# Optimization experiments

Measured on AMD Instinct MI355X. Metric: run time of the kernel, lower is better.

Reference implementation:

```python
import jax, jax.numpy as jnp
import numpy as np

B, L, H = 4096, 4096, 1024  # batch, num_labels, hidden_size


def setup_inputs() -> dict:
    key = jax.random.key(0)
    k1, k2, k3, k4, k5 = jax.random.split(key, 5)
    return {
        "bert_output": jax.random.normal(k1, (B, H), dtype=jnp.float32),
        "label_embed": jax.random.normal(k2, (L, H), dtype=jnp.float32),
        "W": jax.random.normal(k3, (L, H), dtype=jnp.float32) * 0.02,
        "b": jax.random.normal(k4, (L,), dtype=jnp.float32) * 0.02,
        "labels": jax.random.randint(k5, (B, L), 0, 2, dtype=jnp.int32),
    }


def reference(bert_output, label_embed, W, b, labels):
    # Original: output[i, j] = classifier(bert_output[i] + label_embed[j])[j]
    #         = sum_k (x[i,k] + E[j,k]) * W[j,k] + b[j]
    #         = (x @ W^T)[i,j] + (E * W).sum(-1)[j] + b[j]
    xWt = jnp.einsum('bh,lh->bl', bert_output, W)          # [B, L] GEMM
    diag_bias = jnp.sum(label_embed * W, axis=-1) + b       # [L] epilogue
    logits = xWt + diag_bias[None, :]                       # [B, L]
    return logits
```

## Files before the change

kernel.cpp:

```cpp
#include <hip/hip_runtime.h>
#include <hip/hip_bf16.h>

#define Bdim 4096
#define Ldim 4096
#define Hdim 1024
#define TILE 128
#define BK 32

typedef __attribute__((ext_vector_type(8))) __bf16 bf16x8;
typedef __attribute__((ext_vector_type(4))) float floatx4;

__device__ __forceinline__ unsigned short f2bf(float f) {
  union { __hip_bfloat16 h; unsigned short u; } c;
  c.h = __float2bfloat16(f);
  return c.u;
}

__global__ __launch_bounds__(256) void prep_kernel(
    const float* __restrict__ X, const float* __restrict__ E,
    const float* __restrict__ W, const float* __restrict__ b,
    unsigned short* __restrict__ Xb, unsigned short* __restrict__ Wb,
    float* __restrict__ bias) {
  const int blk = blockIdx.x;
  const int t = threadIdx.x;
  if (blk < Ldim) {
    const int row = blk;
    const float4 wv = reinterpret_cast<const float4*>(W + (size_t)row * Hdim)[t];
    const float4 ev = reinterpret_cast<const float4*>(E + (size_t)row * Hdim)[t];
    ushort4 o;
    o.x = f2bf(wv.x); o.y = f2bf(wv.y); o.z = f2bf(wv.z); o.w = f2bf(wv.w);
    reinterpret_cast<ushort4*>(Wb + (size_t)row * Hdim)[t] = o;
    float dot = wv.x * ev.x + wv.y * ev.y + wv.z * ev.z + wv.w * ev.w;
#pragma unroll
    for (int off = 32; off > 0; off >>= 1) dot += __shfl_down(dot, off, 64);
    __shared__ float part[4];
    if ((t & 63) == 0) part[t >> 6] = dot;
    __syncthreads();
    if (t == 0) bias[row] = part[0] + part[1] + part[2] + part[3] + b[row];
  } else {
    const int i = (blk - Ldim) * 256 + t;
    float4 v = reinterpret_cast<const float4*>(X)[i];
    ushort4 o;
    o.x = f2bf(v.x); o.y = f2bf(v.y); o.z = f2bf(v.z); o.w = f2bf(v.w);
    reinterpret_cast<ushort4*>(Xb)[i] = o;
  }
}

__global__ __launch_bounds__(256) void gemm_bias_kernel(
    const unsigned short* __restrict__ A,
    const unsigned short* __restrict__ Bw,
    const float* __restrict__ bias,
    float* __restrict__ C) {
  __shared__ __align__(16) unsigned short ring[3][2][TILE * BK];

  const int tid = threadIdx.x;
  const int wave = tid >> 6;
  const int lane = tid & 63;
  const int m_blk = blockIdx.y * TILE;
  const int n_blk = blockIdx.x * TILE;

  const int srow = wave * 32 + (lane >> 2);
  const unsigned short* gA = A + (size_t)(m_blk + srow) * Hdim + (lane & 3) * 8;
  const unsigned short* gB = Bw + (size_t)(n_blk + srow) * Hdim + (lane & 3) * 8;
  const int lofs = wave * 32 * BK;

  const int wm = (wave >> 1) * 64;
  const int wn = (wave & 1) * 64;
  const int fr = lane & 15;
  const int fq = lane >> 4;
  const int fa = (wm + fr) * BK + fq * 8;
  const int fb = (wn + fr) * BK + fq * 8;

  floatx4 acc[4][4] = {};

#define GLL(src, dst)                                                  \
  __builtin_amdgcn_global_load_lds(                                    \
      (const __attribute__((address_space(1))) void*)(src),            \
      (__attribute__((address_space(3))) void*)(dst), 16, 0, 0)

#define STAGE(slot, kk)                                                \
  do {                                                                 \
    GLL(gA + (kk) * BK, &ring[slot][0][lofs]);                         \
    GLL(gA + (kk) * BK + 16 * Hdim, &ring[slot][0][lofs + 16 * BK]);   \
    GLL(gB + (kk) * BK, &ring[slot][1][lofs]);                         \
    GLL(gB + (kk) * BK + 16 * Hdim, &ring[slot][1][lofs + 16 * BK]);   \
  } while (0)

#define COMPUTE(slot)                                                  \
  do {                                                                 \
    bf16x8 af[4], bfr[4];                                              \
    _Pragma("unroll")                                                  \
    for (int i = 0; i < 4; ++i) {                                      \
      af[i]  = *reinterpret_cast<const bf16x8*>(&ring[slot][0][fa + i * 16 * BK]); \
      bfr[i] = *reinterpret_cast<const bf16x8*>(&ring[slot][1][fb + i * 16 * BK]); \
    }                                                                  \
    _Pragma("unroll")                                                  \
    for (int mi = 0; mi < 4; ++mi)                                     \
      _Pragma("unroll")                                                \
      for (int ni = 0; ni < 4; ++ni)                                   \
        acc[mi][ni] = __builtin_amdgcn_mfma_f32_16x16x32_bf16(         \
            af[mi], bfr[ni], acc[mi][ni], 0, 0, 0);                    \
  } while (0)

#define WAIT4_BAR asm volatile("s_waitcnt vmcnt(4)\n\ts_barrier" ::: "memory")
#define WAIT0_BAR asm volatile("s_waitcnt vmcnt(0)\n\ts_barrier" ::: "memory")

  STAGE(0, 0);
  STAGE(1, 1);

#pragma unroll 1
  for (int kt = 0; kt < 30; kt += 3) {
    WAIT4_BAR;
    STAGE(2, kt + 2);
    COMPUTE(0);
    WAIT4_BAR;
    STAGE(0, kt + 3);
    COMPUTE(1);
    WAIT4_BAR;
    STAGE(1, kt + 4);
    COMPUTE(2);
  }
  WAIT4_BAR;
  COMPUTE(0);
  WAIT0_BAR;
  COMPUTE(1);

#undef GLL
#undef STAGE
#undef COMPUTE
#undef WAIT4_BAR
#undef WAIT0_BAR

  const int col0 = n_blk + wn + fr;
  const int row0 = m_blk + wm + fq * 4;
#pragma unroll
  for (int ni = 0; ni < 4; ++ni) {
    const float bs = bias[col0 + ni * 16];
#pragma unroll
    for (int mi = 0; mi < 4; ++mi) {
      float* cp = C + (size_t)(row0 + mi * 16) * Ldim + (col0 + ni * 16);
      floatx4 v = acc[mi][ni];
      cp[0 * (size_t)Ldim] = v.x + bs;
      cp[1 * (size_t)Ldim] = v.y + bs;
      cp[2 * (size_t)Ldim] = v.z + bs;
      cp[3 * (size_t)Ldim] = v.w + bs;
    }
  }
}

extern "C" void kernel_launch(void* const* d_in, const int* in_sizes, int n_in,
                              void* d_out, int out_size, void* d_ws, size_t ws_size,
                              hipStream_t stream) {
  const float* X = (const float*)d_in[0];
  const float* E = (const float*)d_in[1];
  const float* W = (const float*)d_in[2];
  const float* b = (const float*)d_in[3];
  float* out = (float*)d_out;

  unsigned short* Xb = (unsigned short*)d_ws;
  unsigned short* Wb = Xb + (size_t)Bdim * Hdim;
  float* bias = (float*)(Wb + (size_t)Ldim * Hdim);

  prep_kernel<<<Ldim + Bdim, 256, 0, stream>>>(X, E, W, b, Xb, Wb, bias);
  dim3 grid(Ldim / TILE, Bdim / TILE);
  gemm_bias_kernel<<<grid, 256, 0, stream>>>(Xb, Wb, bias, out);
}
```

Baseline: 57.49 us.

## Enlarge GEMM tile to 256x256x64 with swizzled LDS and interleaved pipeline

Replaces the 128x128x32 triple-buffered GEMM with a 256x256 tile, BK=64, 512 threads, double-buffered LDS, and an XOR swizzle on K offsets to avoid bank conflicts. Loads for the next K-tile are split into quarters interleaved between MFMA quadrants, and setprio raises wave priority during MFMA bursts. This is meant to cut global/LDS traffic per FLOP and hide load latency. The cost is higher register and LDS pressure, one block per CU, and only 256 blocks with no tail slack.

```diff
diff --git a/kernel.cpp b/kernel.cpp
--- a/kernel.cpp
+++ b/kernel.cpp
@@ -4,8 +4,10 @@
 #define Bdim 4096
 #define Ldim 4096
 #define Hdim 1024
-#define TILE 128
-#define BK 32
+#define BM 256
+#define BN 256
+#define BK 64
+#define NT (Hdim / BK)
 
 typedef __attribute__((ext_vector_type(8))) __bf16 bf16x8;
 typedef __attribute__((ext_vector_type(4))) float floatx4;
@@ -46,98 +48,132 @@
   }
 }
 
-__global__ __launch_bounds__(256) void gemm_bias_kernel(
+__global__ __launch_bounds__(512) void gemm_bias_kernel(
     const unsigned short* __restrict__ A,
     const unsigned short* __restrict__ Bw,
     const float* __restrict__ bias,
     float* __restrict__ C) {
-  __shared__ __align__(16) unsigned short ring[3][2][TILE * BK];
+  static_assert(NT >= 3, "pipeline needs >=3 K-tiles");
+  __shared__ __align__(16) unsigned short lds[2][2][BM * BK];
 
   const int tid = threadIdx.x;
   const int wave = tid >> 6;
   const int lane = tid & 63;
-  const int m_blk = blockIdx.y * TILE;
-  const int n_blk = blockIdx.x * TILE;
-
-  const int srow = wave * 32 + (lane >> 2);
-  const unsigned short* gA = A + (size_t)(m_blk + srow) * Hdim + (lane & 3) * 8;
-  const unsigned short* gB = Bw + (size_t)(n_blk + srow) * Hdim + (lane & 3) * 8;
-  const int lofs = wave * 32 * BK;
-
-  const int wm = (wave >> 1) * 64;
-  const int wn = (wave & 1) * 64;
+  const int wm = wave >> 2;
+  const int wn = wave & 3;
+  const int m_blk = blockIdx.y * BM;
+  const int n_blk = blockIdx.x * BN;
+
+  const int srow = wave * 8 + (lane >> 3);
+  const int skofs = ((lane & 7) ^ (lane >> 3)) * 8;
+  const unsigned short* gA = A + (size_t)(m_blk + srow) * Hdim + skofs;
+  const unsigned short* gB = Bw + (size_t)(n_blk + srow) * Hdim + skofs;
+
   const int fr = lane & 15;
   const int fq = lane >> 4;
-  const int fa = (wm + fr) * BK + fq * 8;
-  const int fb = (wn + fr) * BK + fq * 8;
-
-  floatx4 acc[4][4] = {};
+  const int kx0 = ((fq) ^ (fr & 7)) * 8;
+  const int kx1 = ((4 + fq) ^ (fr & 7)) * 8;
+  const int aBase = (wm * 128 + fr) * BK;
+  const int bBase = (wn * 64 + fr) * BK;
+
+  floatx4 acc[8][4] = {};
+  bf16x8 af[8][2], bfv[4][2];
 
 #define GLL(src, dst)                                                  \
   __builtin_amdgcn_global_load_lds(                                    \
       (const __attribute__((address_space(1))) void*)(src),            \
       (__attribute__((address_space(3))) void*)(dst), 16, 0, 0)
 
-#define STAGE(slot, kk)                                                \
-  do {                                                                 \
-    GLL(gA + (kk) * BK, &ring[slot][0][lofs]);                         \
-    GLL(gA + (kk) * BK + 16 * Hdim, &ring[slot][0][lofs + 16 * BK]);   \
-    GLL(gB + (kk) * BK, &ring[slot][1][lofs]);                         \
-    GLL(gB + (kk) * BK + 16 * Hdim, &ring[slot][1][lofs + 16 * BK]);   \
-  } while (0)
-
-#define COMPUTE(slot)                                                  \
-  do {                                                                 \
-    bf16x8 af[4], bfr[4];                                              \
-    _Pragma("unroll")                                                  \
-    for (int i = 0; i < 4; ++i) {                                      \
-      af[i]  = *reinterpret_cast<const bf16x8*>(&ring[slot][0][fa + i * 16 * BK]); \
-      bfr[i] = *reinterpret_cast<const bf16x8*>(&ring[slot][1][fb + i * 16 * BK]); \
-    }                                                                  \
-    _Pragma("unroll")                                                  \
-    for (int mi = 0; mi < 4; ++mi)                                     \
-      _Pragma("unroll")                                                \
-      for (int ni = 0; ni < 4; ++ni)                                   \
+#define STAGE1(c, mat, j, kt)                                          \
+  do {                                                                 \
+    const unsigned short* _g = (mat) ? gB : gA;                        \
+    GLL(_g + (size_t)((j) * 128) * Hdim + (size_t)(kt) * 64,           \
+        &lds[c][mat][((j) * 128 + wave * 8) * BK]);                    \
+    GLL(_g + (size_t)((j) * 128 + 64) * Hdim + (size_t)(kt) * 64,      \
+        &lds[c][mat][((j) * 128 + 64 + wave * 8) * BK]);               \
+  } while (0)
+
+#define READ_R1(c)                                                     \
+  do {                                                                 \
+    _Pragma("unroll") for (int mi = 0; mi < 4; ++mi) {                 \
+      af[mi][0] = *(const bf16x8*)&lds[c][0][aBase + mi * 16 * BK + kx0]; \
+      af[mi][1] = *(const bf16x8*)&lds[c][0][aBase + mi * 16 * BK + kx1]; \
+    }                                                                  \
+    _Pragma("unroll") for (int ni = 0; ni < 2; ++ni) {                 \
+      bfv[ni][0] = *(const bf16x8*)&lds[c][1][bBase + ni * 16 * BK + kx0]; \
+      bfv[ni][1] = *(const bf16x8*)&lds[c][1][bBase + ni * 16 * BK + kx1]; \
+    }                                                                  \
+  } while (0)
+
+#define READ_R2(c)                                                     \
+  do {                                                                 \
+    _Pragma("unroll") for (int mi = 4; mi < 8; ++mi) {                 \
+      af[mi][0] = *(const bf16x8*)&lds[c][0][aBase + mi * 16 * BK + kx0]; \
+      af[mi][1] = *(const bf16x8*)&lds[c][0][aBase + mi * 16 * BK + kx1]; \
+    }                                                                  \
+    _Pragma("unroll") for (int ni = 2; ni < 4; ++ni) {                 \
+      bfv[ni][0] = *(const bf16x8*)&lds[c][1][bBase + ni * 16 * BK + kx0]; \
+      bfv[ni][1] = *(const bf16x8*)&lds[c][1][bBase + ni * 16 * BK + kx1]; \
+    }                                                                  \
+  } while (0)
+
+#define MFMA_Q(M0, N0)                                                 \
+  do {                                                                 \
+    __builtin_amdgcn_s_setprio(1);                                     \
+    _Pragma("unroll") for (int mi = (M0); mi < (M0) + 4; ++mi)         \
+      _Pragma("unroll") for (int ni = (N0); ni < (N0) + 2; ++ni) {     \
         acc[mi][ni] = __builtin_amdgcn_mfma_f32_16x16x32_bf16(         \
-            af[mi], bfr[ni], acc[mi][ni], 0, 0, 0);                    \
-  } while (0)
-
-#define WAIT4_BAR asm volatile("s_waitcnt vmcnt(4)\n\ts_barrier" ::: "memory")
-#define WAIT0_BAR asm volatile("s_waitcnt vmcnt(0)\n\ts_barrier" ::: "memory")
-
-  STAGE(0, 0);
-  STAGE(1, 1);
+            af[mi][0], bfv[ni][0], acc[mi][ni], 0, 0, 0);              \
+        acc[mi][ni] = __builtin_amdgcn_mfma_f32_16x16x32_bf16(         \
+            af[mi][1], bfv[ni][1], acc[mi][ni], 0, 0, 0);              \
+      }                                                                \
+    __builtin_amdgcn_s_setprio(0);                                     \
+  } while (0)
+
+  STAGE1(0, 0, 0, 0);
+  STAGE1(0, 0, 1, 0);
+  STAGE1(0, 1, 0, 0);
+  STAGE1(0, 1, 1, 0);
+  STAGE1(1, 0, 0, 1);
 
 #pragma unroll 1
-  for (int kt = 0; kt < 30; kt += 3) {
-    WAIT4_BAR;
-    STAGE(2, kt + 2);
-    COMPUTE(0);
-    WAIT4_BAR;
-    STAGE(0, kt + 3);
-    COMPUTE(1);
-    WAIT4_BAR;
-    STAGE(1, kt + 4);
-    COMPUTE(2);
+  for (int t = 0; t < NT - 1; ++t) {
+    const int c = t & 1;
+    STAGE1(c ^ 1, 0, 1, t + 1);
+    asm volatile("s_waitcnt vmcnt(4)\n\ts_barrier" ::: "memory");
+    READ_R1(c);
+    MFMA_Q(0, 0);
+    STAGE1(c ^ 1, 1, 0, t + 1);
+    READ_R2(c);
+    MFMA_Q(4, 2);
+    asm volatile("s_barrier" ::: "memory");
+    STAGE1(c ^ 1, 1, 1, t + 1);
+    MFMA_Q(0, 2);
+    if (t < NT - 2) STAGE1(c, 0, 0, t + 2);
+    MFMA_Q(4, 0);
   }
-  WAIT4_BAR;
-  COMPUTE(0);
-  WAIT0_BAR;
-  COMPUTE(1);
+
+  asm volatile("s_waitcnt vmcnt(0)\n\ts_barrier" ::: "memory");
+  READ_R1(1);
+  READ_R2(1);
+  MFMA_Q(0, 0);
+  MFMA_Q(4, 2);
+  MFMA_Q(0, 2);
+  MFMA_Q(4, 0);
 
 #undef GLL
-#undef STAGE
-#undef COMPUTE
-#undef WAIT4_BAR
-#undef WAIT0_BAR
-
-  const int col0 = n_blk + wn + fr;
-  const int row0 = m_blk + wm + fq * 4;
+#undef STAGE1
+#undef READ_R1
+#undef READ_R2
+#undef MFMA_Q
+
+  const int col0 = n_blk + wn * 64 + fr;
+  const int row0 = m_blk + wm * 128 + fq * 4;
 #pragma unroll
   for (int ni = 0; ni < 4; ++ni) {
     const float bs = bias[col0 + ni * 16];
 #pragma unroll
-    for (int mi = 0; mi < 4; ++mi) {
+    for (int mi = 0; mi < 8; ++mi) {
       float* cp = C + (size_t)(row0 + mi * 16) * Ldim + (col0 + ni * 16);
       floatx4 v = acc[mi][ni];
       cp[0 * (size_t)Ldim] = v.x + bs;
@@ -162,6 +198,6 @@
   float* bias = (float*)(Wb + (size_t)Ldim * Hdim);
 
   prep_kernel<<<Ldim + Bdim, 256, 0, stream>>>(X, E, W, b, Xb, Wb, bias);
-  dim3 grid(Ldim / TILE, Bdim / TILE);
-  gemm_bias_kernel<<<grid, 256, 0, stream>>>(Xb, Wb, bias, out);
-}
+  dim3 grid(Ldim / BN, Bdim / BM);
+  gemm_bias_kernel<<<grid, 512, 0, stream>>>(Xb, Wb, bias, out);
+}
```

Result: faster. 52.39 us (-8.9%).

## Use 256x128 tiles with 8 waves, XOR-swizzled LDS, and XCD-aware block mapping

Applied to the files above, without the earlier changes.

The GEMM block grows from 128x128 to 256x128 with 512 threads (8 waves), each wave still computing a 64x64 sub-tile. Each thread now issues three global-to-LDS loads per stage, and the wait count drops to vmcnt(3) to match. The K-chunk offset is XOR-swizzled on both the store and the fragment read to reduce LDS bank conflicts. The 1D grid maps blocks to XCDs so that neighbouring M tiles share a chiplet's L2, improving B-operand reuse. The cost is higher LDS use per block and a launch bound of 4 blocks per CU, which constrains registers.

```diff
diff --git a/kernel.cpp b/kernel.cpp
--- a/kernel.cpp
+++ b/kernel.cpp
@@ -4,8 +4,12 @@
 #define Bdim 4096
 #define Ldim 4096
 #define Hdim 1024
-#define TILE 128
+#define BM 256
+#define BN 128
 #define BK 32
+#define NT (Hdim / BK)
+#define SLOT_B 8192
+#define SLOT_E 12288
 
 typedef __attribute__((ext_vector_type(8))) __bf16 bf16x8;
 typedef __attribute__((ext_vector_type(4))) float floatx4;
@@ -46,30 +50,36 @@
   }
 }
 
-__global__ __launch_bounds__(256) void gemm_bias_kernel(
+__global__ __launch_bounds__(512, 4) void gemm_bias_kernel(
     const unsigned short* __restrict__ A,
     const unsigned short* __restrict__ Bw,
     const float* __restrict__ bias,
     float* __restrict__ C) {
-  __shared__ __align__(16) unsigned short ring[3][2][TILE * BK];
+  __shared__ __align__(16) unsigned short ring[3][SLOT_E];
 
   const int tid = threadIdx.x;
   const int wave = tid >> 6;
   const int lane = tid & 63;
-  const int m_blk = blockIdx.y * TILE;
-  const int n_blk = blockIdx.x * TILE;
+  const int wm = wave >> 1;
+  const int wn = wave & 1;
 
-  const int srow = wave * 32 + (lane >> 2);
-  const unsigned short* gA = A + (size_t)(m_blk + srow) * Hdim + (lane & 3) * 8;
-  const unsigned short* gB = Bw + (size_t)(n_blk + srow) * Hdim + (lane & 3) * 8;
-  const int lofs = wave * 32 * BK;
+  const int bid = blockIdx.x;
+  const int xcd = bid & 7;
+  const int idx = bid >> 3;
+  const int m_blk = (xcd * 2 + (idx & 1)) * BM;
+  const int n_blk = (idx >> 1) * BN;
 
-  const int wm = (wave >> 1) * 64;
-  const int wn = (wave & 1) * 64;
+  const int sr = tid >> 2;
+  const int skofs = ((tid & 3) ^ ((tid >> 3) & 3)) * 8;
+  const unsigned short* gA0 = A + (size_t)(m_blk + sr) * Hdim + skofs;
+  const unsigned short* gA1 = A + (size_t)(m_blk + 128 + sr) * Hdim + skofs;
+  const unsigned short* gB0 = Bw + (size_t)(n_blk + sr) * Hdim + skofs;
+
   const int fr = lane & 15;
   const int fq = lane >> 4;
-  const int fa = (wm + fr) * BK + fq * 8;
-  const int fb = (wn + fr) * BK + fq * 8;
+  const int kx = (fq ^ ((fr >> 1) & 3)) * 8;
+  const int aofs = (wm * 64 + fr) * BK + kx;
+  const int bofs = SLOT_B + (wn * 64 + fr) * BK + kx;
 
   floatx4 acc[4][4] = {};
 
@@ -78,31 +88,30 @@
       (const __attribute__((address_space(1))) void*)(src),            \
       (__attribute__((address_space(3))) void*)(dst), 16, 0, 0)
 
-#define STAGE(slot, kk)                                                \
+#define STAGE(s, kt)                                                   \
   do {                                                                 \
-    GLL(gA + (kk) * BK, &ring[slot][0][lofs]);                         \
-    GLL(gA + (kk) * BK + 16 * Hdim, &ring[slot][0][lofs + 16 * BK]);   \
-    GLL(gB + (kk) * BK, &ring[slot][1][lofs]);                         \
-    GLL(gB + (kk) * BK + 16 * Hdim, &ring[slot][1][lofs + 16 * BK]);   \
+    GLL(gA0 + (size_t)(kt) * BK, &ring[s][tid * 8]);                   \
+    GLL(gA1 + (size_t)(kt) * BK, &ring[s][4096 + tid * 8]);            \
+    GLL(gB0 + (size_t)(kt) * BK, &ring[s][SLOT_B + tid * 8]);          \
   } while (0)
 
-#define COMPUTE(slot)                                                  \
+#define COMPUTE(s)                                                     \
   do {                                                                 \
-    bf16x8 af[4], bfr[4];                                              \
+    bf16x8 af[4], bfv[4];                                              \
     _Pragma("unroll")                                                  \
     for (int i = 0; i < 4; ++i) {                                      \
-      af[i]  = *reinterpret_cast<const bf16x8*>(&ring[slot][0][fa + i * 16 * BK]); \
-      bfr[i] = *reinterpret_cast<const bf16x8*>(&ring[slot][1][fb + i * 16 * BK]); \
+      af[i]  = *(const bf16x8*)&ring[s][aofs + i * 16 * BK];           \
+      bfv[i] = *(const bf16x8*)&ring[s][bofs + i * 16 * BK];           \
     }                                                                  \
     _Pragma("unroll")                                                  \
     for (int mi = 0; mi < 4; ++mi)                                     \
       _Pragma("unroll")                                                \
       for (int ni = 0; ni < 4; ++ni)                                   \
         acc[mi][ni] = __builtin_amdgcn_mfma_f32_16x16x32_bf16(         \
-            af[mi], bfr[ni], acc[mi][ni], 0, 0, 0);                    \
+            af[mi], bfv[ni], acc[mi][ni], 0, 0, 0);                    \
   } while (0)
 
-#define WAIT4_BAR asm volatile("s_waitcnt vmcnt(4)\n\ts_barrier" ::: "memory")
+#define WAIT3_BAR asm volatile("s_waitcnt vmcnt(3)\n\ts_barrier" ::: "memory")
 #define WAIT0_BAR asm volatile("s_waitcnt vmcnt(0)\n\ts_barrier" ::: "memory")
 
   STAGE(0, 0);
@@ -110,17 +119,17 @@
 
 #pragma unroll 1
   for (int kt = 0; kt < 30; kt += 3) {
-    WAIT4_BAR;
+    WAIT3_BAR;
     STAGE(2, kt + 2);
     COMPUTE(0);
-    WAIT4_BAR;
+    WAIT3_BAR;
     STAGE(0, kt + 3);
     COMPUTE(1);
-    WAIT4_BAR;
+    WAIT3_BAR;
     STAGE(1, kt + 4);
     COMPUTE(2);
   }
-  WAIT4_BAR;
+  WAIT3_BAR;
   COMPUTE(0);
   WAIT0_BAR;
   COMPUTE(1);
@@ -128,11 +137,11 @@
 #undef GLL
 #undef STAGE
 #undef COMPUTE
-#undef WAIT4_BAR
+#undef WAIT3_BAR
 #undef WAIT0_BAR
 
-  const int col0 = n_blk + wn + fr;
-  const int row0 = m_blk + wm + fq * 4;
+  const int col0 = n_blk + wn * 64 + fr;
+  const int row0 = m_blk + wm * 64 + fq * 4;
 #pragma unroll
   for (int ni = 0; ni < 4; ++ni) {
     const float bs = bias[col0 + ni * 16];
@@ -162,6 +171,5 @@
   float* bias = (float*)(Wb + (size_t)Ldim * Hdim);
 
   prep_kernel<<<Ldim + Bdim, 256, 0, stream>>>(X, E, W, b, Xb, Wb, bias);
-  dim3 grid(Ldim / TILE, Bdim / TILE);
-  gemm_bias_kernel<<<grid, 256, 0, stream>>>(Xb, Wb, bias, out);
+  gemm_bias_kernel<<<(Bdim / BM) * (Ldim / BN), 512, 0, stream>>>(Xb, Wb, bias, out);
 }
```

After: 54.67 us. 4.9% less time.
